# Performance work log

Hardware: AMD Instinct MI355X
Metric: run time of the kernel (lower is better)

Reference implementation:

```python
import jax, jax.numpy as jnp
import numpy as np
import math

N_EMBD = 1024
N_HEAD = 16
N_LAYER = 12


def setup_inputs() -> dict:
    key = jax.random.key(0)
    kx, kw, kb = jax.random.split(key, 3)
    B, T, C = 4, 2048, N_EMBD
    x = jax.random.normal(kx, (B, T, C), dtype=jnp.float32)
    # nn.Linear(C, 3C): weight [3C, C] scaled by 1/sqrt(2*n_layer), bias [3C]
    bound = 1.0 / math.sqrt(C)
    W = jax.random.uniform(kw, (3 * C, C), minval=-bound, maxval=bound, dtype=jnp.float32)
    W = W * (1.0 / math.sqrt(N_LAYER * 2))
    b = jax.random.uniform(kb, (3 * C,), minval=-bound, maxval=bound, dtype=jnp.float32)
    return {"x": x, "W": W, "b": b}


def reference(x, W, b) -> jnp.ndarray:
    B, T, C = x.shape
    H = N_HEAD
    D = C // H
    qkv = jnp.einsum("btc,oc->bto", x, W) + b  # [B, T, 3C]
    q, k, v = jnp.split(qkv, 3, axis=-1)
    # [B, H, T, D]
    q = q.reshape(B, T, H, D).transpose(0, 2, 1, 3)
    k = k.reshape(B, T, H, D).transpose(0, 2, 1, 3)
    v = v.reshape(B, T, H, D).transpose(0, 2, 1, 3)
    att = jnp.einsum("bhtd,bhsd->bhts", q, k) / math.sqrt(D)  # [B, H, T, T]
    causal = jnp.tril(jnp.ones((T, T), dtype=bool))
    att = jnp.where(causal, att, -jnp.inf)
    att = jax.nn.softmax(att, axis=-1)
    y = jnp.einsum("bhts,bhsd->bhtd", att, v)  # [B, H, T, D]
    return y.transpose(0, 2, 1, 3).reshape(B, T, C)
```

## Files before the change

kernel.cpp:

```cpp
#include <hip/hip_runtime.h>


typedef __attribute__((ext_vector_type(8))) short short8;
typedef __attribute__((ext_vector_type(4))) float f32x4;
typedef __attribute__((ext_vector_type(2))) int int2v;

#define AS1 __attribute__((address_space(1)))
#define AS3 __attribute__((address_space(3)))

__device__ __forceinline__ unsigned short f2bf(float f) {
  unsigned int u = __float_as_uint(f);
  u += 0x7fffu + ((u >> 16) & 1u);
  return (unsigned short)(u >> 16);
}

__device__ __forceinline__ unsigned int pack_bf16(float lo, float hi) {
  return __builtin_amdgcn_perm(__float_as_uint(hi) + 0x8000u,
                               __float_as_uint(lo) + 0x8000u, 0x07060302u);
}

__device__ __forceinline__ void async_copy16(const unsigned short* g, unsigned short* l) {
  const AS1 unsigned char* gp = (const AS1 unsigned char*)(unsigned long long)(uintptr_t)g;
  AS3 unsigned char* lp = (AS3 unsigned char*)(unsigned int)(uintptr_t)l;
  __builtin_amdgcn_global_load_lds((const AS1 void*)gp, (AS3 void*)lp, 16, 0, 0);
}

__global__ __launch_bounds__(256) void cvt_both(const float* __restrict__ x,
                                                const float* __restrict__ W,
                                                unsigned short* __restrict__ xt,
                                                unsigned short* __restrict__ wt) {
  int U = blockIdx.x * 256 + threadIdx.x;
  const float* in;
  unsigned short* out;
  if (U < 1048576) { in = x; out = xt; }
  else             { in = W; out = wt; U -= 1048576; }
  int u6 = U & 63, frag = (U >> 6) & 15, kt = (U >> 10) & 15, bt = U >> 14;
  int ks = frag & 1, i = (frag >> 1) & 3, half = frag >> 3;
  int row = bt * 128 + half * 64 + i * 16 + (u6 & 15);
  int colf = kt * 64 + ks * 32 + (u6 >> 4) * 8;
  const float4* p = (const float4*)(in + (size_t)row * 1024 + colf);
  float4 a = p[0], b = p[1];
  uint4 o;
  o.x = pack_bf16(a.x, a.y);
  o.y = pack_bf16(a.z, a.w);
  o.z = pack_bf16(b.x, b.y);
  o.w = pack_bf16(b.z, b.w);
  *(uint4*)(out + (size_t)U * 8) = o;
}

__global__ __launch_bounds__(256) void qkv_gemm(const unsigned short* __restrict__ xt,
                                                const unsigned short* __restrict__ wt,
                                                const float* __restrict__ bias,
                                                unsigned short* __restrict__ qb,
                                                unsigned short* __restrict__ kvb) {
  __shared__ unsigned short As[3][4096];
  __shared__ unsigned short Bs[3][4096];
  int tid = threadIdx.x;
  int wave = tid >> 6, lane = tid & 63;
  int q4 = lane >> 4, l16 = lane & 15;
  int bm = blockIdx.x, bn = blockIdx.y;

  f32x4 zero = {0.f, 0.f, 0.f, 0.f};
  f32x4 acc[4][4];
#pragma unroll
  for (int i = 0; i < 4; ++i)
#pragma unroll
    for (int j = 0; j < 4; ++j) acc[i][j] = zero;

  const unsigned short* Abase = xt + (size_t)bm * 16 * 8192;
  const unsigned short* Bbase = wt + (size_t)bn * 16 * 8192;

  auto stage = [&](int d, int kt32) {
    int kt64 = kt32 >> 1, ks = kt32 & 1;
    const unsigned short* ga = Abase + (size_t)kt64 * 8192;
    const unsigned short* gb = Bbase + (size_t)kt64 * 8192;
#pragma unroll
    for (int j = 0; j < 2; ++j) {
      int fi = wave * 2 + j;
      int f = (fi >> 2) * 8 + (fi & 3) * 2 + ks;
      async_copy16(ga + f * 512 + lane * 8, &As[d][fi * 512]);
      async_copy16(gb + f * 512 + lane * 8, &Bs[d][fi * 512]);
    }
  };

  auto compute = [&](const unsigned short* Ac, const unsigned short* Bc) {
    short8 af[4], bf[4];
#pragma unroll
    for (int i = 0; i < 4; ++i)
      af[i] = *(const short8*)(Ac + ((wave & 1) * 4 + i) * 512 + lane * 8);
#pragma unroll
    for (int j = 0; j < 4; ++j)
      bf[j] = *(const short8*)(Bc + ((wave >> 1) * 4 + j) * 512 + lane * 8);
#pragma unroll
    for (int i = 0; i < 4; ++i)
#pragma unroll
      for (int j = 0; j < 4; ++j)
        acc[i][j] = __builtin_amdgcn_mfma_f32_16x16x32_bf16(af[i], bf[j], acc[i][j], 0, 0, 0);
  };

  stage(0, 0);
  stage(1, 1);
  int cur = 0, nxt2 = 2;
  for (int kt = 0; kt < 31; ++kt) {
    asm volatile("s_waitcnt vmcnt(4)\n\ts_barrier" ::: "memory");
    if (kt < 30) stage(nxt2, kt + 2);
    compute(As[cur], Bs[cur]);
    cur = cur == 2 ? 0 : cur + 1;
    nxt2 = nxt2 == 2 ? 0 : nxt2 + 1;
  }
  asm volatile("s_waitcnt vmcnt(0)\n\ts_barrier" ::: "memory");
  compute(As[cur], Bs[cur]);

  const float QSCALE = 0.18033688011112042f;
  int rowbase = bm * 128 + (wave & 1) * 64;
  int colbase = bn * 128 + (wave >> 1) * 64;
#pragma unroll
  for (int j = 0; j < 4; ++j) {
    int o = colbase + j * 16 + l16;
    float bv = bias[o];
#pragma unroll
    for (int i = 0; i < 4; ++i) {
      int r0 = rowbase + i * 16 + q4 * 4;
      int b = r0 >> 11, t0 = r0 & 2047;
      if (o < 1024) {
        int h = o >> 6, d = o & 63;
#pragma unroll
        for (int r = 0; r < 4; ++r)
          qb[((((size_t)b * 16 + h) * 2048 + t0 + r) << 6) + d] =
              f2bf((acc[i][j][r] + bv) * QSCALE);
      } else if (o < 2048) {
        int o2 = o - 1024;
        int h = o2 >> 6, dd = o2 & 63;
        int st = t0 >> 6, s6 = t0 & 63;
        int ns = s6 >> 4, l16p = s6 & 15;
        int ks = dd >> 5, q4p = (dd & 31) >> 3, jj = dd & 7;
        size_t base = ((size_t)(b * 16 + h) * 32 + st) * 8192 +
                      ((ns * 2 + ks) * 64 + q4p * 16 + l16p) * 8 + jj;
#pragma unroll
        for (int r = 0; r < 4; ++r)
          kvb[base + r * 8] = f2bf(acc[i][j][r] + bv);
      } else {
        int o3 = o - 2048;
        int h = o3 >> 6, dd = o3 & 63;
        int st = t0 >> 6, s6 = t0 & 63;
        int a = s6 >> 5, q4p = (s6 >> 3) & 3, j0 = s6 & 7;
        int nd = dd >> 4, l16p = dd & 15;
        size_t base = ((size_t)(b * 16 + h) * 32 + st) * 8192 + 4096 +
                      (size_t)(((a * 4 + nd) * 64 + q4p * 16 + l16p) * 8 + j0);
        ushort4 pk;
        pk.x = f2bf(acc[i][j][0] + bv);
        pk.y = f2bf(acc[i][j][1] + bv);
        pk.z = f2bf(acc[i][j][2] + bv);
        pk.w = f2bf(acc[i][j][3] + bv);
        *(ushort4*)(&kvb[base]) = pk;
      }
    }
  }
}

__global__ __launch_bounds__(128, 3) void flash_attn(const unsigned short* __restrict__ qb,
                                                     const unsigned short* __restrict__ kvb,
                                                     float* __restrict__ out) {
  __shared__ unsigned short buf[2][8192];

  const int tid = threadIdx.x;
  const int wave = tid >> 6, lane = tid & 63;
  const int q4 = lane >> 4, l16 = lane & 15;
  const int n = blockIdx.x;
  const int bh = (n & 7) * 8 + ((n >> 3) & 7);
  const int bx = n >> 6;
  const int b = bh >> 4, h = bh & 15;

  const unsigned short* Qg = qb + (size_t)bh * (2048 * 64);
  const unsigned short* KVg = kvb + (size_t)bh * 32 * 8192;
  union { unsigned int u[4]; short8 s8; } ones_u;
  ones_u.u[0] = 0x3F803F80u; ones_u.u[1] = 0x3F803F80u;
  ones_u.u[2] = 0x3F803F80u; ones_u.u[3] = 0x3F803F80u;
  const short8 ones8 = ones_u.s8;

  auto stage = [&](int d, int st) {
    const unsigned short* tp = KVg + (size_t)st * 8192;
#pragma unroll
    for (int i2 = 0; i2 < 8; ++i2) {
      int u = i2 * 128 + wave * 64;
      async_copy16(tp + (u + lane) * 8, &buf[d][u * 8]);
    }
  };

  for (int pass = 0; pass < 2; ++pass) {
    const int qt = pass ? 31 - bx : bx;
    const int t0w = qt * 64 + wave * 32;

    short8 qf[2][2];
#pragma unroll
    for (int mt = 0; mt < 2; ++mt)
#pragma unroll
      for (int ks = 0; ks < 2; ++ks)
        qf[mt][ks] = *(const short8*)(Qg + (size_t)(t0w + mt * 16 + l16) * 64 +
                                      ks * 32 + q4 * 8);

    f32x4 zero = {0.f, 0.f, 0.f, 0.f};
    f32x4 oT[2][4];
#pragma unroll
    for (int mt = 0; mt < 2; ++mt)
#pragma unroll
      for (int nd = 0; nd < 4; ++nd) oT[mt][nd] = zero;
    f32x4 l_acc[2] = {zero, zero};

    __syncthreads();
    stage(0, 0);
    for (int st = 0; st <= qt; ++st) {
      __syncthreads();
      if (st < qt) stage((st + 1) & 1, st + 1);
      const unsigned short* cur = buf[st & 1];

      f32x4 sT[2][4];
#pragma unroll
      for (int ns = 0; ns < 4; ++ns) {
        short8 kf0 = *(const short8*)(cur + (ns * 2 + 0) * 512 + lane * 8);
        short8 kf1 = *(const short8*)(cur + (ns * 2 + 1) * 512 + lane * 8);
#pragma unroll
        for (int mt = 0; mt < 2; ++mt) {
          sT[mt][ns] = __builtin_amdgcn_mfma_f32_16x16x32_bf16(kf0, qf[mt][0], zero, 0, 0, 0);
          sT[mt][ns] = __builtin_amdgcn_mfma_f32_16x16x32_bf16(kf1, qf[mt][1], sT[mt][ns], 0, 0, 0);
        }
      }

      if (st == qt) {
#pragma unroll
        for (int mt = 0; mt < 2; ++mt) {
          int tg = t0w + mt * 16 + l16;
#pragma unroll
          for (int ns = 0; ns < 4; ++ns) {
            int sgb = st * 64 + ns * 16 + q4 * 4;
#pragma unroll
            for (int r = 0; r < 4; ++r)
              if (sgb + r > tg) sT[mt][ns][r] = -3.0e38f;
          }
        }
      }

#pragma unroll
      for (int a = 0; a < 2; ++a) {
        short8 pfrag[2];
#pragma unroll
        for (int mt = 0; mt < 2; ++mt) {
          unsigned int e0 = pack_bf16(__builtin_amdgcn_exp2f(sT[mt][2 * a][0]),
                                      __builtin_amdgcn_exp2f(sT[mt][2 * a][1]));
          unsigned int e1 = pack_bf16(__builtin_amdgcn_exp2f(sT[mt][2 * a][2]),
                                      __builtin_amdgcn_exp2f(sT[mt][2 * a][3]));
          unsigned int o0 = pack_bf16(__builtin_amdgcn_exp2f(sT[mt][2 * a + 1][0]),
                                      __builtin_amdgcn_exp2f(sT[mt][2 * a + 1][1]));
          unsigned int o1 = pack_bf16(__builtin_amdgcn_exp2f(sT[mt][2 * a + 1][2]),
                                      __builtin_amdgcn_exp2f(sT[mt][2 * a + 1][3]));
          int2v r0 = __builtin_amdgcn_permlane32_swap((int)e0, (int)o0, false, false);
          int2v r1 = __builtin_amdgcn_permlane32_swap((int)e1, (int)o1, false, false);
          int2v s0 = __builtin_amdgcn_permlane16_swap(r0.x, r0.y, false, false);
          int2v s1 = __builtin_amdgcn_permlane16_swap(r1.x, r1.y, false, false);
          union { int w[4]; short8 s8; } pu;
          pu.w[0] = s0.x;
          pu.w[1] = s1.x;
          pu.w[2] = s0.y;
          pu.w[3] = s1.y;
          pfrag[mt] = pu.s8;
        }
#pragma unroll
        for (int nd = 0; nd < 4; ++nd) {
          short8 vf = *(const short8*)(cur + 4096 + ((a * 4 + nd) * 64 + lane) * 8);
#pragma unroll
          for (int mt = 0; mt < 2; ++mt)
            oT[mt][nd] = __builtin_amdgcn_mfma_f32_16x16x32_bf16(vf, pfrag[mt], oT[mt][nd], 0, 0, 0);
        }
#pragma unroll
        for (int mt = 0; mt < 2; ++mt)
          l_acc[mt] = __builtin_amdgcn_mfma_f32_16x16x32_bf16(ones8, pfrag[mt], l_acc[mt], 0, 0, 0);
      }
    }

#pragma unroll
    for (int mt = 0; mt < 2; ++mt) {
      float inv = 1.0f / l_acc[mt][0];
      int t = t0w + mt * 16 + l16;
      float* op = out + (size_t)(b * 2048 + t) * 1024 + h * 64 + q4 * 4;
#pragma unroll
      for (int nd = 0; nd < 4; ++nd) {
        float4 o4 = {oT[mt][nd][0] * inv, oT[mt][nd][1] * inv,
                     oT[mt][nd][2] * inv, oT[mt][nd][3] * inv};
        *(float4*)(op + nd * 16) = o4;
      }
    }
  }
}

extern "C" void kernel_launch(void* const* d_in, const int* in_sizes, int n_in,
                              void* d_out, int out_size, void* d_ws, size_t ws_size,
                              hipStream_t stream) {
  const float* x = (const float*)d_in[0];
  const float* W = (const float*)d_in[1];
  const float* bias = (const float*)d_in[2];
  float* out = (float*)d_out;

  char* ws = (char*)d_ws;
  unsigned short* xt = (unsigned short*)(ws);
  unsigned short* wt = (unsigned short*)(ws + 16777216);
  unsigned short* qb = (unsigned short*)(ws + 23068672);
  unsigned short* kvb = (unsigned short*)(ws + 39845888);

  hipLaunchKernelGGL(cvt_both, dim3(5632), dim3(256), 0, stream, x, W, xt, wt);
  hipLaunchKernelGGL(qkv_gemm, dim3(64, 24), dim3(256), 0, stream, xt, wt, bias,
                     qb, kvb);
  hipLaunchKernelGGL(flash_attn, dim3(1024), dim3(128), 0, stream, qb, kvb, out);
}
```

Baseline: 211.3 us.

## Software-pipeline QK^T of next tile with PV of current tile, split K/V staging

Splits K and V tile staging into separate async copies and restructures the attention loop so that the QK^T and exp for tile st+1 are issued right after the PV accumulation of tile st. K is prefetched two tiles ahead and V one tile ahead. The aim is to give the scheduler independent MFMA and exp work to interleave and to hide LDS load latency. It also raises wave priority with s_setprio around the compute. In exchange the P fragments now stay live across iterations, which raises register pressure, and the K/V buffer reuse relies on careful barrier placement.

```diff
diff --git a/kernel.cpp b/kernel.cpp
--- a/kernel.cpp
+++ b/kernel.cpp
@@ -178,12 +178,20 @@
   ones_u.u[2] = 0x3F803F80u; ones_u.u[3] = 0x3F803F80u;
   const short8 ones8 = ones_u.s8;
 
-  auto stage = [&](int d, int st) {
+  auto stageK = [&](int d, int st) {
     const unsigned short* tp = KVg + (size_t)st * 8192;
 #pragma unroll
-    for (int i2 = 0; i2 < 8; ++i2) {
+    for (int i2 = 0; i2 < 4; ++i2) {
       int u = i2 * 128 + wave * 64;
       async_copy16(tp + (u + lane) * 8, &buf[d][u * 8]);
+    }
+  };
+  auto stageV = [&](int d, int st) {
+    const unsigned short* tp = KVg + (size_t)st * 8192 + 4096;
+#pragma unroll
+    for (int i2 = 0; i2 < 4; ++i2) {
+      int u = i2 * 128 + wave * 64;
+      async_copy16(tp + (u + lane) * 8, &buf[d][4096 + u * 8]);
     }
   };
 
@@ -206,43 +214,35 @@
 #pragma unroll
       for (int nd = 0; nd < 4; ++nd) oT[mt][nd] = zero;
     f32x4 l_acc[2] = {zero, zero};
-
-    __syncthreads();
-    stage(0, 0);
-    for (int st = 0; st <= qt; ++st) {
-      __syncthreads();
-      if (st < qt) stage((st + 1) & 1, st + 1);
-      const unsigned short* cur = buf[st & 1];
-
+    short8 pf[2][2];
+
+    auto qkt_build = [&](const unsigned short* kp, int tile) {
       f32x4 sT[2][4];
 #pragma unroll
       for (int ns = 0; ns < 4; ++ns) {
-        short8 kf0 = *(const short8*)(cur + (ns * 2 + 0) * 512 + lane * 8);
-        short8 kf1 = *(const short8*)(cur + (ns * 2 + 1) * 512 + lane * 8);
+        short8 kf0 = *(const short8*)(kp + (ns * 2 + 0) * 512 + lane * 8);
+        short8 kf1 = *(const short8*)(kp + (ns * 2 + 1) * 512 + lane * 8);
 #pragma unroll
         for (int mt = 0; mt < 2; ++mt) {
           sT[mt][ns] = __builtin_amdgcn_mfma_f32_16x16x32_bf16(kf0, qf[mt][0], zero, 0, 0, 0);
           sT[mt][ns] = __builtin_amdgcn_mfma_f32_16x16x32_bf16(kf1, qf[mt][1], sT[mt][ns], 0, 0, 0);
         }
       }
-
-      if (st == qt) {
+      if (tile == qt) {
 #pragma unroll
         for (int mt = 0; mt < 2; ++mt) {
           int tg = t0w + mt * 16 + l16;
 #pragma unroll
           for (int ns = 0; ns < 4; ++ns) {
-            int sgb = st * 64 + ns * 16 + q4 * 4;
+            int sgb = qt * 64 + ns * 16 + q4 * 4;
 #pragma unroll
             for (int r = 0; r < 4; ++r)
               if (sgb + r > tg) sT[mt][ns][r] = -3.0e38f;
           }
         }
       }
-
-#pragma unroll
-      for (int a = 0; a < 2; ++a) {
-        short8 pfrag[2];
+#pragma unroll
+      for (int a = 0; a < 2; ++a)
 #pragma unroll
         for (int mt = 0; mt < 2; ++mt) {
           unsigned int e0 = pack_bf16(__builtin_amdgcn_exp2f(sT[mt][2 * a][0]),
@@ -262,20 +262,46 @@
           pu.w[1] = s1.x;
           pu.w[2] = s0.y;
           pu.w[3] = s1.y;
-          pfrag[mt] = pu.s8;
+          pf[a][mt] = pu.s8;
         }
+    };
+
+    auto pv = [&](const unsigned short* vp) {
+#pragma unroll
+      for (int a = 0; a < 2; ++a) {
 #pragma unroll
         for (int nd = 0; nd < 4; ++nd) {
-          short8 vf = *(const short8*)(cur + 4096 + ((a * 4 + nd) * 64 + lane) * 8);
+          short8 vf = *(const short8*)(vp + ((a * 4 + nd) * 64 + lane) * 8);
 #pragma unroll
           for (int mt = 0; mt < 2; ++mt)
-            oT[mt][nd] = __builtin_amdgcn_mfma_f32_16x16x32_bf16(vf, pfrag[mt], oT[mt][nd], 0, 0, 0);
+            oT[mt][nd] = __builtin_amdgcn_mfma_f32_16x16x32_bf16(vf, pf[a][mt], oT[mt][nd], 0, 0, 0);
         }
 #pragma unroll
         for (int mt = 0; mt < 2; ++mt)
-          l_acc[mt] = __builtin_amdgcn_mfma_f32_16x16x32_bf16(ones8, pfrag[mt], l_acc[mt], 0, 0, 0);
-      }
-    }
+          l_acc[mt] = __builtin_amdgcn_mfma_f32_16x16x32_bf16(ones8, pf[a][mt], l_acc[mt], 0, 0, 0);
+      }
+    };
+
+    __syncthreads();
+    stageK(0, 0);
+    stageV(0, 0);
+    if (qt >= 1) stageK(1, 1);
+    __syncthreads();
+    qkt_build(buf[0], 0);
+
+    for (int st = 0; st < qt; ++st) {
+      __syncthreads();
+      if (st + 2 <= qt) stageK(st & 1, st + 2);
+      stageV((st + 1) & 1, st + 1);
+      __builtin_amdgcn_s_setprio(1);
+      pv(buf[st & 1] + 4096);
+      qkt_build(buf[(st + 1) & 1], st + 1);
+      __builtin_amdgcn_s_setprio(0);
+    }
+    __syncthreads();
+    __builtin_amdgcn_s_setprio(1);
+    pv(buf[qt & 1] + 4096);
+    __builtin_amdgcn_s_setprio(0);
 
 #pragma unroll
     for (int mt = 0; mt < 2; ++mt) {
```

After: 206.0 us. 2.5% less time.
